# Kernel optimization log

Hardware: AMD Instinct MI355X
Metric: run time of the kernel (lower is better)

## Reference

```python
import jax, jax.numpy as jnp
import numpy as np

EMBED_DIM = 1024
NUM_HEADS = 16
HEAD_DIM = EMBED_DIM // NUM_HEADS
BZ, Q_LEN, CACHE_LEN = 4, 512, 1536


def setup_inputs() -> dict:
    key = jax.random.key(0)
    ks = jax.random.split(key, 8)
    inp = {
        "hidden_states": jax.random.normal(ks[0], (BZ, Q_LEN, EMBED_DIM), jnp.float32),
        "attention_mask": jnp.zeros((BZ, 1, 1, CACHE_LEN + Q_LEN), jnp.float32),
        "k_cache": jax.random.normal(ks[1], (BZ, CACHE_LEN, EMBED_DIM), jnp.float32),
        "v_cache": jax.random.normal(ks[2], (BZ, CACHE_LEN, EMBED_DIM), jnp.float32),
        "Wq": jax.random.normal(ks[3], (EMBED_DIM, EMBED_DIM), jnp.float32) * 0.02,
        "bq": jnp.zeros((EMBED_DIM,), jnp.float32),
        "Wk": jax.random.normal(ks[4], (EMBED_DIM, EMBED_DIM), jnp.float32) * 0.02,
        "bk": jnp.zeros((EMBED_DIM,), jnp.float32),
        "Wv": jax.random.normal(ks[5], (EMBED_DIM, EMBED_DIM), jnp.float32) * 0.02,
        "bv": jnp.zeros((EMBED_DIM,), jnp.float32),
        "Wo": jax.random.normal(ks[6], (EMBED_DIM, EMBED_DIM), jnp.float32) * 0.02,
        "bo": jnp.zeros((EMBED_DIM,), jnp.float32),
    }
    return inp


def reference(hidden_states, attention_mask, k_cache, v_cache,
              Wq, bq, Wk, bk, Wv, bv, Wo, bo):
    bz, q_len, embed_dim = hidden_states.shape
    # projections (nn.Linear: x @ W.T + b)
    q = hidden_states @ Wq.T + bq
    k_new = hidden_states @ Wk.T + bk
    v_new = hidden_states @ Wv.T + bv
    # KV-cache concat (self_attn path)
    k = jnp.concatenate([k_cache, k_new], axis=1)  # [bz, kv_len, E]
    v = jnp.concatenate([v_cache, v_new], axis=1)
    q_begin = k_cache.shape[1]
    kv_len = k.shape[1]
    # split heads -> [bz, H, L, D]
    qh = q.reshape(bz, q_len, NUM_HEADS, HEAD_DIM).transpose(0, 2, 1, 3)
    kh = k.reshape(bz, kv_len, NUM_HEADS, HEAD_DIM).transpose(0, 2, 1, 3)
    vh = v.reshape(bz, kv_len, NUM_HEADS, HEAD_DIM).transpose(0, 2, 1, 3)
    scores = jnp.einsum("bhqd,bhkd->bhqk", qh, kh) / (HEAD_DIM ** 0.5)
    # causal mask slice causal_mask[q_begin:q_begin+q_len, :kv_len]
    rows = q_begin + jnp.arange(q_len)          # absolute query positions
    cols = jnp.arange(kv_len)
    causal = jnp.where(cols[None, :] > rows[:, None], -jnp.inf, 0.0).astype(scores.dtype)
    scores = scores + attention_mask + causal
    probs = jax.nn.softmax(scores, axis=-1)
    ctx = jnp.einsum("bhqk,bhkd->bhqd", probs, vh)
    ctx = ctx.transpose(0, 2, 1, 3).reshape(bz, q_len, embed_dim)
    out = ctx @ Wo.T + bo
    return out, k, v
```

## Files before the change

### kernel.cpp

```cpp
#include <hip/hip_runtime.h>
#include <hip/hip_bf16.h>
#include <stdint.h>

#define BZv 4
#define QL 512
#define CL 1536
#define KVL 2048
#define EMB 1024
#define NH 16
#define HD 64
#define QSCALE 0.18033688011112042f

typedef __attribute__((ext_vector_type(8))) short short8;
typedef __attribute__((ext_vector_type(4))) float floatx4;

__device__ __forceinline__ unsigned short f2b(float f) {
  union { float f; unsigned int u; } v; v.f = f;
  return (unsigned short)((v.u + 0x7FFFu + ((v.u >> 16) & 1u)) >> 16);
}

__device__ __forceinline__ ushort2 pk2(float a, float b) {
  union { __hip_bfloat162 h; ushort2 u; } c;
  c.h = __float22bfloat162_rn(make_float2(a, b));
  return c.u;
}

#if __has_builtin(__builtin_amdgcn_exp2f)
#define EXP2F(x) __builtin_amdgcn_exp2f(x)
#else
#define EXP2F(x) exp2f(x)
#endif

__device__ __forceinline__ void gload_lds16(const void* g, void* l) {
  __builtin_amdgcn_global_load_lds(
      (const __attribute__((address_space(1))) unsigned char*)g,
      (__attribute__((address_space(3))) unsigned char*)l, 16, 0, 0);
}

__global__ __launch_bounds__(256) void prep_kernel(
    const float* __restrict__ hid, const float* __restrict__ Wq, const float* __restrict__ Wk,
    const float* __restrict__ Wv, const float* __restrict__ Wo,
    const float* __restrict__ kc, const float* __restrict__ vc, const float* __restrict__ msk,
    unsigned short* __restrict__ Xb, unsigned short* __restrict__ Wqb, unsigned short* __restrict__ Wkb,
    unsigned short* __restrict__ Wvb, unsigned short* __restrict__ Wob,
    unsigned short* __restrict__ Kb, unsigned short* __restrict__ Vb,
    float* __restrict__ kf, float* __restrict__ vf, unsigned short* __restrict__ wb)
{
  const long HID4 = (long)BZv * QL * EMB / 4;
  const long W4   = (long)EMB * EMB / 4;
  const long C4   = (long)BZv * CL * EMB / 4;
  const long t0 = HID4, t1 = t0 + W4, t2 = t1 + W4, t3 = t2 + W4, t4 = t3 + W4;
  const long t5 = t4 + C4, t6 = t5 + C4;
  const long total = t6 + (long)BZv * KVL / 4;
  for (long i = (long)blockIdx.x * blockDim.x + threadIdx.x; i < total;
       i += (long)gridDim.x * blockDim.x) {
    if (i < t4) {
      const float* src; unsigned short* dst; long j;
      if (i < t0)      { src = hid; dst = Xb;  j = i; }
      else if (i < t1) { src = Wq;  dst = Wqb; j = i - t0; }
      else if (i < t2) { src = Wk;  dst = Wkb; j = i - t1; }
      else if (i < t3) { src = Wv;  dst = Wvb; j = i - t2; }
      else             { src = Wo;  dst = Wob; j = i - t3; }
      float4 v = ((const float4*)src)[j];
      ushort4 o; o.x = f2b(v.x); o.y = f2b(v.y); o.z = f2b(v.z); o.w = f2b(v.w);
      ((ushort4*)dst)[j] = o;
    } else if (i < t6) {
      bool isV = (i >= t5);
      long j = i - (isV ? t5 : t4);
      const float* src = isV ? vc : kc;
      float4 v = ((const float4*)src)[j];
      long e4 = j * 4;
      int b = (int)(e4 / ((long)CL * EMB));
      long rem = e4 - (long)b * CL * EMB;
      long doff = (long)b * KVL * EMB + rem;
      if (isV) {
        *((float4*)(vf + doff)) = v;
        int row = (int)(rem >> 10);
        float w = __expf(msk[b * KVL + row]);
        ushort4 o; o.x = f2b(v.x * w); o.y = f2b(v.y * w);
        o.z = f2b(v.z * w); o.w = f2b(v.w * w);
        *((ushort4*)(Vb + doff)) = o;
      } else {
        *((float4*)(kf + doff)) = v;
        ushort4 o; o.x = f2b(v.x); o.y = f2b(v.y); o.z = f2b(v.z); o.w = f2b(v.w);
        *((ushort4*)(Kb + doff)) = o;
      }
    } else {
      long j = i - t6;
      float4 m4 = ((const float4*)msk)[j];
      ushort4 o;
      o.x = f2b(__expf(m4.x)); o.y = f2b(__expf(m4.y));
      o.z = f2b(__expf(m4.z)); o.w = f2b(__expf(m4.w));
      ((ushort4*)wb)[j] = o;
    }
  }
}

__global__ __launch_bounds__(256) void qkv_gemm(
    const unsigned short* __restrict__ Xb,
    const unsigned short* __restrict__ Wqb, const unsigned short* __restrict__ Wkb,
    const unsigned short* __restrict__ Wvb,
    const float* __restrict__ bq, const float* __restrict__ bk, const float* __restrict__ bv,
    const float* __restrict__ msk,
    unsigned short* __restrict__ Qb, unsigned short* __restrict__ Kb, unsigned short* __restrict__ Vb,
    float* __restrict__ kf, float* __restrict__ vf)
{
  __shared__ unsigned short At[128 * 32];
  __shared__ unsigned short Bt[64 * 32];
  const int tid = threadIdx.x, lane = tid & 63, wave = tid >> 6;
  const int quad = lane >> 4, l = lane & 15;
  const int mat = blockIdx.x >> 4;
  const int ncol = (blockIdx.x & 15) * 64;
  const int mbase = blockIdx.y * 128;
  const unsigned short* W = (mat == 0) ? Wqb : (mat == 1) ? Wkb : Wvb;
  const float* bias = (mat == 0) ? bq : (mat == 1) ? bk : bv;
  const int srow = tid >> 2, slds = tid & 3;
  const int rh = wave * 32;

  floatx4 zero = {0.f, 0.f, 0.f, 0.f};
  floatx4 acc[2][4];
#pragma unroll
  for (int i = 0; i < 2; i++)
#pragma unroll
    for (int j = 0; j < 4; j++) acc[i][j] = zero;

  for (int k0 = 0; k0 < EMB; k0 += 32) {
    __syncthreads();
#pragma unroll
    for (int s = 0; s < 2; s++) {
      int row = s * 64 + srow;
      int gc = slds ^ (row & 3);
      gload_lds16(Xb + (size_t)(mbase + row) * EMB + k0 + gc * 8, &At[row * 32 + slds * 8]);
    }
    {
      int row = srow;
      int gc = slds ^ (row & 3);
      gload_lds16(W + (size_t)(ncol + row) * EMB + k0 + gc * 8, &Bt[row * 32 + slds * 8]);
    }
    __syncthreads();
    short8 af[2], bfr[4];
#pragma unroll
    for (int rt = 0; rt < 2; rt++) {
      int row = rh + rt * 16 + l;
      af[rt] = *(const short8*)&At[row * 32 + ((quad ^ (row & 3)) * 8)];
    }
#pragma unroll
    for (int ct = 0; ct < 4; ct++) {
      int row = ct * 16 + l;
      bfr[ct] = *(const short8*)&Bt[row * 32 + ((quad ^ (row & 3)) * 8)];
    }
#pragma unroll
    for (int rt = 0; rt < 2; rt++)
#pragma unroll
      for (int ct = 0; ct < 4; ct++)
        acc[rt][ct] = __builtin_amdgcn_mfma_f32_16x16x32_bf16(af[rt], bfr[ct], acc[rt][ct], 0, 0, 0);
  }

#pragma unroll
  for (int ct = 0; ct < 4; ct++) {
    int col = ncol + ct * 16 + l;
    float bb = bias[col];
#pragma unroll
    for (int rt = 0; rt < 2; rt++)
#pragma unroll
      for (int r = 0; r < 4; r++) {
        int m = mbase + rh + rt * 16 + quad * 4 + r;
        float val = acc[rt][ct][r] + bb;
        if (mat == 0) {
          Qb[(size_t)m * EMB + col] = f2b(val * QSCALE);
        } else {
          size_t a = ((size_t)(m >> 9) * KVL + CL + (m & 511)) * EMB + col;
          if (mat == 1) { Kb[a] = f2b(val); kf[a] = val; }
          else {
            float w = __expf(msk[(m >> 9) * KVL + CL + (m & 511)]);
            Vb[a] = f2b(val * w); vf[a] = val;
          }
        }
      }
  }
}

__global__ __launch_bounds__(256) void oproj_gemm(
    const unsigned short* __restrict__ A, const unsigned short* __restrict__ W,
    const float* __restrict__ bias, float* __restrict__ out)
{
  __shared__ unsigned short At[64 * 32];
  __shared__ unsigned short Bt[64 * 32];
  const int tid = threadIdx.x, lane = tid & 63, wave = tid >> 6;
  const int quad = lane >> 4, l = lane & 15;
  const int ncol = blockIdx.x * 64;
  const int mbase = blockIdx.y * 64;
  const int srow = tid >> 2, slds = tid & 3;
  const int rh = (wave & 1) * 32, ch = (wave >> 1) * 32;

  floatx4 zero = {0.f, 0.f, 0.f, 0.f};
  floatx4 acc[2][2];
#pragma unroll
  for (int i = 0; i < 2; i++)
#pragma unroll
    for (int j = 0; j < 2; j++) acc[i][j] = zero;

  for (int k0 = 0; k0 < EMB; k0 += 32) {
    __syncthreads();
    {
      int gc = slds ^ (srow & 3);
      gload_lds16(A + (size_t)(mbase + srow) * EMB + k0 + gc * 8, &At[srow * 32 + slds * 8]);
      gload_lds16(W + (size_t)(ncol + srow) * EMB + k0 + gc * 8, &Bt[srow * 32 + slds * 8]);
    }
    __syncthreads();
    short8 af[2], bfr[2];
#pragma unroll
    for (int rt = 0; rt < 2; rt++) {
      int row = rh + rt * 16 + l;
      af[rt] = *(const short8*)&At[row * 32 + ((quad ^ (row & 3)) * 8)];
    }
#pragma unroll
    for (int ct = 0; ct < 2; ct++) {
      int row = ch + ct * 16 + l;
      bfr[ct] = *(const short8*)&Bt[row * 32 + ((quad ^ (row & 3)) * 8)];
    }
#pragma unroll
    for (int rt = 0; rt < 2; rt++)
#pragma unroll
      for (int ct = 0; ct < 2; ct++)
        acc[rt][ct] = __builtin_amdgcn_mfma_f32_16x16x32_bf16(af[rt], bfr[ct], acc[rt][ct], 0, 0, 0);
  }

#pragma unroll
  for (int ct = 0; ct < 2; ct++) {
    int col = ncol + ch + ct * 16 + l;
    float bb = bias[col];
#pragma unroll
    for (int rt = 0; rt < 2; rt++)
#pragma unroll
      for (int r = 0; r < 4; r++) {
        int m = mbase + rh + rt * 16 + quad * 4 + r;
        out[(size_t)m * EMB + col] = acc[rt][ct][r] + bb;
      }
  }
}

__global__ __launch_bounds__(256) void attn_kernel(
    const unsigned short* __restrict__ Qb, const unsigned short* __restrict__ Kb,
    const unsigned short* __restrict__ Vb, const unsigned short* __restrict__ wb,
    unsigned short* __restrict__ Cb)
{
  __shared__ unsigned short Vt[2][66 * 72];
  __shared__ unsigned short Pl[4][16 * 72];
  const int id = blockIdx.x;
  const int hb = id & 63, qt = id >> 6;
  const int b = hb >> 4, h = hb & 15;
  const int tid = threadIdx.x, lane = tid & 63, wave = tid >> 6;
  const int quad = lane >> 4, l = lane & 15;
  const int qbase = qt * 64 + wave * 16;

  const unsigned short* qp = Qb + (size_t)(b * QL + qbase + l) * EMB + h * HD + quad * 8;
  const short8 bq0 = *(const short8*)qp;
  const short8 bq1 = *(const short8*)(qp + 32);

  floatx4 zero = {0.f, 0.f, 0.f, 0.f};
  floatx4 o[4], o4 = zero;
#pragma unroll
  for (int c = 0; c < 4; c++) o[c] = zero;
  float mr = -INFINITY;

  const int kv_end = CL + qt * 64 + 64;
  const int vp = tid & 31, vg = tid >> 5;
  const unsigned short* vsrc = Vb + (size_t)(b * KVL) * EMB + h * HD + vg * 8;
  const unsigned short* wsrc = wb + (size_t)b * KVL + 2 * vp;
  const unsigned short* kbase = Kb + (size_t)(b * KVL) * EMB + h * HD + quad * 8;

  uint4 va = *(const uint4*)(vsrc + (size_t)(2 * vp) * EMB);
  uint4 vbr = *(const uint4*)(vsrc + (size_t)(2 * vp + 1) * EMB);
  short8 kc[8];
#pragma unroll
  for (int c = 0; c < 4; c++) {
    const unsigned short* kp = kbase + (size_t)(c * 16 + l) * EMB;
    kc[2 * c] = *(const short8*)kp;
    kc[2 * c + 1] = *(const short8*)(kp + 32);
  }
  {
    const unsigned short* pa = (const unsigned short*)&va;
    const unsigned short* pb = (const unsigned short*)&vbr;
#pragma unroll
    for (int j = 0; j < 8; j++) {
      ushort2 t; t.x = pa[j]; t.y = pb[j];
      *(ushort2*)&Vt[0][(vg * 8 + j) * 72 + 2 * vp] = t;
    }
    if (vg == 0) *(ushort2*)&Vt[0][64 * 72 + 2 * vp] = *(const ushort2*)wsrc;
  }
  __syncthreads();

  int cur = 0;
  for (int kv0 = 0; kv0 < kv_end; kv0 += 64) {
    const bool more = (kv0 + 64 < kv_end);
    uint4 vna, vnb; ushort2 wn; short8 kn[8];
    if (more) {
      const unsigned short* vs = vsrc + (size_t)(kv0 + 64 + 2 * vp) * EMB;
      vna = *(const uint4*)vs;
      vnb = *(const uint4*)(vs + EMB);
      if (vg == 0) wn = *(const ushort2*)(wsrc + kv0 + 64);
#pragma unroll
      for (int c = 0; c < 4; c++) {
        const unsigned short* kp = kbase + (size_t)(kv0 + 64 + c * 16 + l) * EMB;
        kn[2 * c] = *(const short8*)kp;
        kn[2 * c + 1] = *(const short8*)(kp + 32);
      }
    }
    floatx4 s[4];
#pragma unroll
    for (int c = 0; c < 4; c++) {
      s[c] = __builtin_amdgcn_mfma_f32_16x16x32_bf16(kc[2 * c], bq0, zero, 0, 0, 0);
      s[c] = __builtin_amdgcn_mfma_f32_16x16x32_bf16(kc[2 * c + 1], bq1, s[c], 0, 0, 0);
    }
    if (kv0 + 63 > CL + qbase) {
      const int lim = CL + qbase + l;
#pragma unroll
      for (int c = 0; c < 4; c++) {
        int kvb = kv0 + c * 16 + quad * 4;
#pragma unroll
        for (int r = 0; r < 4; r++)
          s[c][r] = (kvb + r <= lim) ? s[c][r] : -INFINITY;
      }
    }
    float t0 = fmaxf(fmaxf(s[0][0], s[0][1]), fmaxf(s[0][2], s[0][3]));
    float t1 = fmaxf(fmaxf(s[1][0], s[1][1]), fmaxf(s[1][2], s[1][3]));
    float t2 = fmaxf(fmaxf(s[2][0], s[2][1]), fmaxf(s[2][2], s[2][3]));
    float t3 = fmaxf(fmaxf(s[3][0], s[3][1]), fmaxf(s[3][2], s[3][3]));
    float lmax = fmaxf(fmaxf(t0, t1), fmaxf(t2, t3));
    lmax = fmaxf(lmax, __shfl_xor(lmax, 16, 64));
    lmax = fmaxf(lmax, __shfl_xor(lmax, 32, 64));
    float mnew = fmaxf(mr, lmax);
    float alpha = EXP2F(mr - mnew);
    mr = mnew;
#pragma unroll
    for (int c = 0; c < 4; c++) {
      float p0 = EXP2F(s[c][0] - mnew), p1 = EXP2F(s[c][1] - mnew);
      float p2 = EXP2F(s[c][2] - mnew), p3 = EXP2F(s[c][3] - mnew);
      ushort2 lo = pk2(p0, p1), hi = pk2(p2, p3);
      ushort4 pk; pk.x = lo.x; pk.y = lo.y; pk.z = hi.x; pk.w = hi.y;
      *(ushort4*)&Pl[wave][l * 72 + c * 16 + quad * 4] = pk;
    }
#pragma unroll
    for (int c = 0; c < 4; c++)
#pragma unroll
      for (int r = 0; r < 4; r++) o[c][r] *= alpha;
#pragma unroll
    for (int r = 0; r < 4; r++) o4[r] *= alpha;
    asm volatile("s_waitcnt lgkmcnt(0)" ::: "memory");
    short8 pf0 = *(const short8*)&Pl[wave][l * 72 + quad * 8];
    short8 pf1 = *(const short8*)&Pl[wave][l * 72 + 32 + quad * 8];
    short8 vw0 = *(const short8*)&Vt[cur][64 * 72 + quad * 8];
    short8 vw1 = *(const short8*)&Vt[cur][64 * 72 + 32 + quad * 8];
    o4 = __builtin_amdgcn_mfma_f32_16x16x32_bf16(vw0, pf0, o4, 0, 0, 0);
    o4 = __builtin_amdgcn_mfma_f32_16x16x32_bf16(vw1, pf1, o4, 0, 0, 0);
#pragma unroll
    for (int c = 0; c < 4; c++) {
      short8 a0v = *(const short8*)&Vt[cur][(c * 16 + l) * 72 + quad * 8];
      short8 a1v = *(const short8*)&Vt[cur][(c * 16 + l) * 72 + 32 + quad * 8];
      o[c] = __builtin_amdgcn_mfma_f32_16x16x32_bf16(a0v, pf0, o[c], 0, 0, 0);
      o[c] = __builtin_amdgcn_mfma_f32_16x16x32_bf16(a1v, pf1, o[c], 0, 0, 0);
    }
    if (more) {
      const unsigned short* pa = (const unsigned short*)&vna;
      const unsigned short* pb = (const unsigned short*)&vnb;
#pragma unroll
      for (int j = 0; j < 8; j++) {
        ushort2 t; t.x = pa[j]; t.y = pb[j];
        *(ushort2*)&Vt[cur ^ 1][(vg * 8 + j) * 72 + 2 * vp] = t;
      }
      if (vg == 0) *(ushort2*)&Vt[cur ^ 1][64 * 72 + 2 * vp] = wn;
#pragma unroll
      for (int i = 0; i < 8; i++) kc[i] = kn[i];
    }
    __syncthreads();
    cur ^= 1;
  }

  float inv = 1.0f / o4[0];
  size_t qrow = (size_t)(b * QL + qbase + l) * EMB + h * HD;
#pragma unroll
  for (int c = 0; c < 4; c++)
#pragma unroll
    for (int r = 0; r < 4; r++)
      Cb[qrow + c * 16 + quad * 4 + r] = f2b(o[c][r] * inv);
}

extern "C" void kernel_launch(void* const* d_in, const int* in_sizes, int n_in,
                              void* d_out, int out_size, void* d_ws, size_t ws_size,
                              hipStream_t stream) {
  const float* hid  = (const float*)d_in[0];
  const float* mask = (const float*)d_in[1];
  const float* kc   = (const float*)d_in[2];
  const float* vc   = (const float*)d_in[3];
  const float* Wq   = (const float*)d_in[4];
  const float* bq   = (const float*)d_in[5];
  const float* Wk   = (const float*)d_in[6];
  const float* bk   = (const float*)d_in[7];
  const float* Wv   = (const float*)d_in[8];
  const float* bv   = (const float*)d_in[9];
  const float* Wo   = (const float*)d_in[10];
  const float* bo   = (const float*)d_in[11];

  float* out_f = (float*)d_out;
  float* kf = out_f + (size_t)BZv * QL * EMB;
  float* vf = kf + (size_t)BZv * KVL * EMB;

  char* p = (char*)d_ws;
  unsigned short* Xb  = (unsigned short*)p; p += (size_t)BZv * QL * EMB * 2;
  unsigned short* Wqb = (unsigned short*)p; p += (size_t)EMB * EMB * 2;
  unsigned short* Wkb = (unsigned short*)p; p += (size_t)EMB * EMB * 2;
  unsigned short* Wvb = (unsigned short*)p; p += (size_t)EMB * EMB * 2;
  unsigned short* Wob = (unsigned short*)p; p += (size_t)EMB * EMB * 2;
  unsigned short* Qb  = (unsigned short*)p; p += (size_t)BZv * QL * EMB * 2;
  unsigned short* Kb  = (unsigned short*)p; p += (size_t)BZv * KVL * EMB * 2;
  unsigned short* Vb  = (unsigned short*)p; p += (size_t)BZv * KVL * EMB * 2;
  unsigned short* Cb  = (unsigned short*)p; p += (size_t)BZv * QL * EMB * 2;
  unsigned short* wbp = (unsigned short*)p; p += (size_t)BZv * KVL * 2;

  prep_kernel<<<2048, 256, 0, stream>>>(hid, Wq, Wk, Wv, Wo, kc, vc, mask,
                                        Xb, Wqb, Wkb, Wvb, Wob, Kb, Vb, kf, vf, wbp);
  qkv_gemm<<<dim3(48, 16), 256, 0, stream>>>(Xb, Wqb, Wkb, Wvb, bq, bk, bv, mask,
                                             Qb, Kb, Vb, kf, vf);
  attn_kernel<<<512, 256, 0, stream>>>(Qb, Kb, Vb, wbp, Cb);
  oproj_gemm<<<dim3(16, 32), 256, 0, stream>>>(Cb, Wob, bo, out_f);
}
```

Baseline: 287.8 us.

## Split-KV attention across waves, pre-transpose V, enlarge GEMM tiles

Attention now gives each block 16 query rows and splits the KV tiles across its four waves. Partial results are merged through shared memory with a log-sum-exp style rescale, which raises the grid from 512 to 2048 blocks. A new vtrans_kernel writes V (plus the mask-weight row) transposed per head into global memory, so the attention loop loads V fragments straight from global instead of transposing through LDS. The QKV and output-projection GEMMs move to larger 128-wide N tiles for more reuse. The costs are an extra kernel launch, an extra V round trip through memory, and more registers per thread.

New measurement: 325.8 us. 1.13x slower.

```diff
diff --git a/kernel.cpp b/kernel.cpp
--- a/kernel.cpp
+++ b/kernel.cpp
@@ -106,21 +106,21 @@
     float* __restrict__ kf, float* __restrict__ vf)
 {
   __shared__ unsigned short At[128 * 32];
-  __shared__ unsigned short Bt[64 * 32];
+  __shared__ unsigned short Bt[128 * 32];
   const int tid = threadIdx.x, lane = tid & 63, wave = tid >> 6;
   const int quad = lane >> 4, l = lane & 15;
-  const int mat = blockIdx.x >> 4;
-  const int ncol = (blockIdx.x & 15) * 64;
+  const int mat = blockIdx.x >> 3;
+  const int ncol = (blockIdx.x & 7) * 128;
   const int mbase = blockIdx.y * 128;
   const unsigned short* W = (mat == 0) ? Wqb : (mat == 1) ? Wkb : Wvb;
   const float* bias = (mat == 0) ? bq : (mat == 1) ? bk : bv;
   const int srow = tid >> 2, slds = tid & 3;
-  const int rh = wave * 32;
+  const int rh = (wave & 1) * 64, ch = (wave >> 1) * 64;
 
   floatx4 zero = {0.f, 0.f, 0.f, 0.f};
-  floatx4 acc[2][4];
-#pragma unroll
-  for (int i = 0; i < 2; i++)
+  floatx4 acc[4][4];
+#pragma unroll
+  for (int i = 0; i < 4; i++)
 #pragma unroll
     for (int j = 0; j < 4; j++) acc[i][j] = zero;
 
@@ -132,51 +132,88 @@
       int gc = slds ^ (row & 3);
       gload_lds16(Xb + (size_t)(mbase + row) * EMB + k0 + gc * 8, &At[row * 32 + slds * 8]);
     }
-    {
-      int row = srow;
+#pragma unroll
+    for (int s = 0; s < 2; s++) {
+      int row = s * 64 + srow;
       int gc = slds ^ (row & 3);
       gload_lds16(W + (size_t)(ncol + row) * EMB + k0 + gc * 8, &Bt[row * 32 + slds * 8]);
     }
     __syncthreads();
-    short8 af[2], bfr[4];
-#pragma unroll
-    for (int rt = 0; rt < 2; rt++) {
+    short8 af[4], bfr[4];
+#pragma unroll
+    for (int rt = 0; rt < 4; rt++) {
       int row = rh + rt * 16 + l;
       af[rt] = *(const short8*)&At[row * 32 + ((quad ^ (row & 3)) * 8)];
     }
 #pragma unroll
     for (int ct = 0; ct < 4; ct++) {
-      int row = ct * 16 + l;
+      int row = ch + ct * 16 + l;
       bfr[ct] = *(const short8*)&Bt[row * 32 + ((quad ^ (row & 3)) * 8)];
     }
 #pragma unroll
-    for (int rt = 0; rt < 2; rt++)
+    for (int rt = 0; rt < 4; rt++)
 #pragma unroll
       for (int ct = 0; ct < 4; ct++)
         acc[rt][ct] = __builtin_amdgcn_mfma_f32_16x16x32_bf16(af[rt], bfr[ct], acc[rt][ct], 0, 0, 0);
   }
 
 #pragma unroll
-  for (int ct = 0; ct < 4; ct++) {
-    int col = ncol + ct * 16 + l;
-    float bb = bias[col];
-#pragma unroll
-    for (int rt = 0; rt < 2; rt++)
-#pragma unroll
-      for (int r = 0; r < 4; r++) {
-        int m = mbase + rh + rt * 16 + quad * 4 + r;
-        float val = acc[rt][ct][r] + bb;
+  for (int rt = 0; rt < 4; rt++)
+#pragma unroll
+    for (int r = 0; r < 4; r++) {
+      int m = mbase + rh + rt * 16 + quad * 4 + r;
+      size_t orow; float w = 1.f;
+      if (mat == 0) orow = (size_t)m;
+      else {
+        orow = (size_t)(m >> 9) * KVL + CL + (m & 511);
+        if (mat == 2) w = __expf(msk[orow]);
+      }
+#pragma unroll
+      for (int ct = 0; ct < 4; ct++) {
+        int col = ncol + ch + ct * 16 + l;
+        float val = acc[rt][ct][r] + bias[col];
         if (mat == 0) {
           Qb[(size_t)m * EMB + col] = f2b(val * QSCALE);
         } else {
-          size_t a = ((size_t)(m >> 9) * KVL + CL + (m & 511)) * EMB + col;
+          size_t a = orow * EMB + col;
           if (mat == 1) { Kb[a] = f2b(val); kf[a] = val; }
-          else {
-            float w = __expf(msk[(m >> 9) * KVL + CL + (m & 511)]);
-            Vb[a] = f2b(val * w); vf[a] = val;
-          }
+          else          { Vb[a] = f2b(val * w); vf[a] = val; }
         }
       }
+    }
+}
+
+__global__ __launch_bounds__(256) void vtrans_kernel(
+    const unsigned short* __restrict__ Vb, const unsigned short* __restrict__ wb,
+    unsigned short* __restrict__ Vtg)
+{
+  __shared__ unsigned short T[64 * 72];
+  const int id = blockIdx.x;
+  const int bh = id & 63, kt = id >> 6;
+  const int b = bh >> 4, h = bh & 15;
+  const int kv0 = kt * 64;
+  const int tid = threadIdx.x;
+  {
+    const int r = tid >> 2, dbase = (tid & 3) * 16;
+    const unsigned short* src = Vb + (size_t)(b * KVL + kv0 + r) * EMB + h * HD + dbase;
+    uint4 lo = *(const uint4*)src;
+    uint4 hi = *(const uint4*)(src + 8);
+    *(uint4*)&T[r * 72 + dbase] = lo;
+    *(uint4*)&T[r * 72 + dbase + 8] = hi;
+  }
+  __syncthreads();
+  {
+    const int d = tid >> 2, kcv = (tid & 3) * 16;
+    unsigned short tmp[16];
+#pragma unroll
+    for (int j = 0; j < 16; j++) tmp[j] = T[(kcv + j) * 72 + d];
+    unsigned short* dst = Vtg + ((size_t)bh * 65 + d) * KVL + kv0 + kcv;
+    *(uint4*)dst = *(const uint4*)&tmp[0];
+    *(uint4*)(dst + 8) = *(const uint4*)&tmp[8];
+  }
+  if (tid < 16) {
+    ushort4 wv = *(const ushort4*)(wb + (size_t)b * KVL + kv0 + tid * 4);
+    *(ushort4*)(Vtg + ((size_t)bh * 65 + 64) * KVL + kv0 + tid * 4) = wv;
   }
 }
 
@@ -185,49 +222,54 @@
     const float* __restrict__ bias, float* __restrict__ out)
 {
   __shared__ unsigned short At[64 * 32];
-  __shared__ unsigned short Bt[64 * 32];
+  __shared__ unsigned short Bt[128 * 32];
   const int tid = threadIdx.x, lane = tid & 63, wave = tid >> 6;
   const int quad = lane >> 4, l = lane & 15;
-  const int ncol = blockIdx.x * 64;
+  const int ncol = blockIdx.x * 128;
   const int mbase = blockIdx.y * 64;
   const int srow = tid >> 2, slds = tid & 3;
-  const int rh = (wave & 1) * 32, ch = (wave >> 1) * 32;
+  const int rh = (wave & 1) * 32, ch = (wave >> 1) * 64;
 
   floatx4 zero = {0.f, 0.f, 0.f, 0.f};
-  floatx4 acc[2][2];
+  floatx4 acc[2][4];
 #pragma unroll
   for (int i = 0; i < 2; i++)
 #pragma unroll
-    for (int j = 0; j < 2; j++) acc[i][j] = zero;
+    for (int j = 0; j < 4; j++) acc[i][j] = zero;
 
   for (int k0 = 0; k0 < EMB; k0 += 32) {
     __syncthreads();
     {
       int gc = slds ^ (srow & 3);
       gload_lds16(A + (size_t)(mbase + srow) * EMB + k0 + gc * 8, &At[srow * 32 + slds * 8]);
-      gload_lds16(W + (size_t)(ncol + srow) * EMB + k0 + gc * 8, &Bt[srow * 32 + slds * 8]);
+    }
+#pragma unroll
+    for (int s = 0; s < 2; s++) {
+      int row = s * 64 + srow;
+      int gc = slds ^ (row & 3);
+      gload_lds16(W + (size_t)(ncol + row) * EMB + k0 + gc * 8, &Bt[row * 32 + slds * 8]);
     }
     __syncthreads();
-    short8 af[2], bfr[2];
+    short8 af[2], bfr[4];
 #pragma unroll
     for (int rt = 0; rt < 2; rt++) {
       int row = rh + rt * 16 + l;
       af[rt] = *(const short8*)&At[row * 32 + ((quad ^ (row & 3)) * 8)];
     }
 #pragma unroll
-    for (int ct = 0; ct < 2; ct++) {
+    for (int ct = 0; ct < 4; ct++) {
       int row = ch + ct * 16 + l;
       bfr[ct] = *(const short8*)&Bt[row * 32 + ((quad ^ (row & 3)) * 8)];
     }
 #pragma unroll
     for (int rt = 0; rt < 2; rt++)
 #pragma unroll
-      for (int ct = 0; ct < 2; ct++)
+      for (int ct = 0; ct < 4; ct++)
         acc[rt][ct] = __builtin_amdgcn_mfma_f32_16x16x32_bf16(af[rt], bfr[ct], acc[rt][ct], 0, 0, 0);
   }
 
 #pragma unroll
-  for (int ct = 0; ct < 2; ct++) {
+  for (int ct = 0; ct < 4; ct++) {
     int col = ncol + ch + ct * 16 + l;
     float bb = bias[col];
 #pragma unroll
@@ -242,79 +284,57 @@
 
 __global__ __launch_bounds__(256) void attn_kernel(
     const unsigned short* __restrict__ Qb, const unsigned short* __restrict__ Kb,
-    const unsigned short* __restrict__ Vb, const unsigned short* __restrict__ wb,
-    unsigned short* __restrict__ Cb)
+    const unsigned short* __restrict__ Vtg, unsigned short* __restrict__ Cb)
 {
-  __shared__ unsigned short Vt[2][66 * 72];
   __shared__ unsigned short Pl[4][16 * 72];
+  __shared__ float cmb[4][16][68];
   const int id = blockIdx.x;
-  const int hb = id & 63, qt = id >> 6;
-  const int b = hb >> 4, h = hb & 15;
+  const int bh = id & 63, qt = id >> 6;
+  const int b = bh >> 4, h = bh & 15;
   const int tid = threadIdx.x, lane = tid & 63, wave = tid >> 6;
   const int quad = lane >> 4, l = lane & 15;
-  const int qbase = qt * 64 + wave * 16;
-
-  const unsigned short* qp = Qb + (size_t)(b * QL + qbase + l) * EMB + h * HD + quad * 8;
+  const int q0 = qt * 16;
+
+  const unsigned short* qp = Qb + (size_t)(b * QL + q0 + l) * EMB + h * HD + quad * 8;
   const short8 bq0 = *(const short8*)qp;
   const short8 bq1 = *(const short8*)(qp + 32);
 
+  const unsigned short* kbase = Kb + (size_t)(b * KVL) * EMB + h * HD + quad * 8;
+  const unsigned short* vtb = Vtg + (size_t)bh * 65 * KVL;
+
   floatx4 zero = {0.f, 0.f, 0.f, 0.f};
   floatx4 o[4], o4 = zero;
 #pragma unroll
   for (int c = 0; c < 4; c++) o[c] = zero;
   float mr = -INFINITY;
 
-  const int kv_end = CL + qt * 64 + 64;
-  const int vp = tid & 31, vg = tid >> 5;
-  const unsigned short* vsrc = Vb + (size_t)(b * KVL) * EMB + h * HD + vg * 8;
-  const unsigned short* wsrc = wb + (size_t)b * KVL + 2 * vp;
-  const unsigned short* kbase = Kb + (size_t)(b * KVL) * EMB + h * HD + quad * 8;
-
-  uint4 va = *(const uint4*)(vsrc + (size_t)(2 * vp) * EMB);
-  uint4 vbr = *(const uint4*)(vsrc + (size_t)(2 * vp + 1) * EMB);
-  short8 kc[8];
-#pragma unroll
-  for (int c = 0; c < 4; c++) {
-    const unsigned short* kp = kbase + (size_t)(c * 16 + l) * EMB;
-    kc[2 * c] = *(const short8*)kp;
-    kc[2 * c + 1] = *(const short8*)(kp + 32);
-  }
-  {
-    const unsigned short* pa = (const unsigned short*)&va;
-    const unsigned short* pb = (const unsigned short*)&vbr;
-#pragma unroll
-    for (int j = 0; j < 8; j++) {
-      ushort2 t; t.x = pa[j]; t.y = pb[j];
-      *(ushort2*)&Vt[0][(vg * 8 + j) * 72 + 2 * vp] = t;
-    }
-    if (vg == 0) *(ushort2*)&Vt[0][64 * 72 + 2 * vp] = *(const ushort2*)wsrc;
-  }
-  __syncthreads();
-
-  int cur = 0;
-  for (int kv0 = 0; kv0 < kv_end; kv0 += 64) {
-    const bool more = (kv0 + 64 < kv_end);
-    uint4 vna, vnb; ushort2 wn; short8 kn[8];
-    if (more) {
-      const unsigned short* vs = vsrc + (size_t)(kv0 + 64 + 2 * vp) * EMB;
-      vna = *(const uint4*)vs;
-      vnb = *(const uint4*)(vs + EMB);
-      if (vg == 0) wn = *(const ushort2*)(wsrc + kv0 + 64);
-#pragma unroll
-      for (int c = 0; c < 4; c++) {
-        const unsigned short* kp = kbase + (size_t)(kv0 + 64 + c * 16 + l) * EMB;
-        kn[2 * c] = *(const short8*)kp;
-        kn[2 * c + 1] = *(const short8*)(kp + 32);
-      }
-    }
+  const int kv_end = CL + q0 + 16;
+  const int ntiles = (kv_end + 63) >> 6;
+
+  for (int t = wave; t < ntiles; t += 4) {
+    const int kv0 = t * 64;
+    short8 kc0[4], kc1[4], av0[4], av1[4];
+#pragma unroll
+    for (int c = 0; c < 4; c++) {
+      const unsigned short* kp = kbase + (size_t)(kv0 + c * 16 + l) * EMB;
+      kc0[c] = *(const short8*)kp;
+      kc1[c] = *(const short8*)(kp + 32);
+      const unsigned short* vpr = vtb + (size_t)(c * 16 + l) * KVL + kv0 + quad * 8;
+      av0[c] = *(const short8*)vpr;
+      av1[c] = *(const short8*)(vpr + 32);
+    }
+    const unsigned short* wpr = vtb + (size_t)64 * KVL + kv0 + quad * 8;
+    const short8 vw0 = *(const short8*)wpr;
+    const short8 vw1 = *(const short8*)(wpr + 32);
+
     floatx4 s[4];
 #pragma unroll
     for (int c = 0; c < 4; c++) {
-      s[c] = __builtin_amdgcn_mfma_f32_16x16x32_bf16(kc[2 * c], bq0, zero, 0, 0, 0);
-      s[c] = __builtin_amdgcn_mfma_f32_16x16x32_bf16(kc[2 * c + 1], bq1, s[c], 0, 0, 0);
-    }
-    if (kv0 + 63 > CL + qbase) {
-      const int lim = CL + qbase + l;
+      s[c] = __builtin_amdgcn_mfma_f32_16x16x32_bf16(kc0[c], bq0, zero, 0, 0, 0);
+      s[c] = __builtin_amdgcn_mfma_f32_16x16x32_bf16(kc1[c], bq1, s[c], 0, 0, 0);
+    }
+    if (kv0 + 63 >= kv_end) {
+      const int lim = CL + q0 + l;
 #pragma unroll
       for (int c = 0; c < 4; c++) {
         int kvb = kv0 + c * 16 + quad * 4;
@@ -350,40 +370,41 @@
     asm volatile("s_waitcnt lgkmcnt(0)" ::: "memory");
     short8 pf0 = *(const short8*)&Pl[wave][l * 72 + quad * 8];
     short8 pf1 = *(const short8*)&Pl[wave][l * 72 + 32 + quad * 8];
-    short8 vw0 = *(const short8*)&Vt[cur][64 * 72 + quad * 8];
-    short8 vw1 = *(const short8*)&Vt[cur][64 * 72 + 32 + quad * 8];
     o4 = __builtin_amdgcn_mfma_f32_16x16x32_bf16(vw0, pf0, o4, 0, 0, 0);
     o4 = __builtin_amdgcn_mfma_f32_16x16x32_bf16(vw1, pf1, o4, 0, 0, 0);
 #pragma unroll
     for (int c = 0; c < 4; c++) {
-      short8 a0v = *(const short8*)&Vt[cur][(c * 16 + l) * 72 + quad * 8];
-      short8 a1v = *(const short8*)&Vt[cur][(c * 16 + l) * 72 + 32 + quad * 8];
-      o[c] = __builtin_amdgcn_mfma_f32_16x16x32_bf16(a0v, pf0, o[c], 0, 0, 0);
-      o[c] = __builtin_amdgcn_mfma_f32_16x16x32_bf16(a1v, pf1, o[c], 0, 0, 0);
-    }
-    if (more) {
-      const unsigned short* pa = (const unsigned short*)&vna;
-      const unsigned short* pb = (const unsigned short*)&vnb;
-#pragma unroll
-      for (int j = 0; j < 8; j++) {
-        ushort2 t; t.x = pa[j]; t.y = pb[j];
-        *(ushort2*)&Vt[cur ^ 1][(vg * 8 + j) * 72 + 2 * vp] = t;
-      }
-      if (vg == 0) *(ushort2*)&Vt[cur ^ 1][64 * 72 + 2 * vp] = wn;
-#pragma unroll
-      for (int i = 0; i < 8; i++) kc[i] = kn[i];
-    }
-    __syncthreads();
-    cur ^= 1;
-  }
-
-  float inv = 1.0f / o4[0];
-  size_t qrow = (size_t)(b * QL + qbase + l) * EMB + h * HD;
+      o[c] = __builtin_amdgcn_mfma_f32_16x16x32_bf16(av0[c], pf0, o[c], 0, 0, 0);
+      o[c] = __builtin_amdgcn_mfma_f32_16x16x32_bf16(av1[c], pf1, o[c], 0, 0, 0);
+    }
+  }
+
 #pragma unroll
   for (int c = 0; c < 4; c++)
-#pragma unroll
-    for (int r = 0; r < 4; r++)
-      Cb[qrow + c * 16 + quad * 4 + r] = f2b(o[c][r] * inv);
+    *(float4*)&cmb[wave][l][c * 16 + quad * 4] = *(float4*)&o[c];
+  if (quad == 0) { cmb[wave][l][64] = mr; cmb[wave][l][65] = o4[0]; }
+  __syncthreads();
+
+  {
+    const int q = tid >> 4, dc = (tid & 15) * 4;
+    float m0 = cmb[0][q][64], m1 = cmb[1][q][64], m2 = cmb[2][q][64], m3 = cmb[3][q][64];
+    float mstar = fmaxf(fmaxf(m0, m1), fmaxf(m2, m3));
+    float s0 = EXP2F(m0 - mstar), s1 = EXP2F(m1 - mstar);
+    float s2 = EXP2F(m2 - mstar), s3 = EXP2F(m3 - mstar);
+    float den = s0 * cmb[0][q][65] + s1 * cmb[1][q][65] +
+                s2 * cmb[2][q][65] + s3 * cmb[3][q][65];
+    float4 a0 = *(float4*)&cmb[0][q][dc];
+    float4 a1 = *(float4*)&cmb[1][q][dc];
+    float4 a2 = *(float4*)&cmb[2][q][dc];
+    float4 a3 = *(float4*)&cmb[3][q][dc];
+    float inv = 1.0f / den;
+    float r0 = (s0 * a0.x + s1 * a1.x + s2 * a2.x + s3 * a3.x) * inv;
+    float r1 = (s0 * a0.y + s1 * a1.y + s2 * a2.y + s3 * a3.y) * inv;
+    float r2 = (s0 * a0.z + s1 * a1.z + s2 * a2.z + s3 * a3.z) * inv;
+    float r3 = (s0 * a0.w + s1 * a1.w + s2 * a2.w + s3 * a3.w) * inv;
+    ushort4 outv; outv.x = f2b(r0); outv.y = f2b(r1); outv.z = f2b(r2); outv.w = f2b(r3);
+    *(ushort4*)(Cb + (size_t)(b * QL + q0 + q) * EMB + h * HD + dc) = outv;
+  }
 }
 
 extern "C" void kernel_launch(void* const* d_in, const int* in_sizes, int n_in,
@@ -417,11 +438,13 @@
   unsigned short* Vb  = (unsigned short*)p; p += (size_t)BZv * KVL * EMB * 2;
   unsigned short* Cb  = (unsigned short*)p; p += (size_t)BZv * QL * EMB * 2;
   unsigned short* wbp = (unsigned short*)p; p += (size_t)BZv * KVL * 2;
+  unsigned short* Vtg = (unsigned short*)p; p += (size_t)NH * BZv * 65 * KVL * 2;
 
   prep_kernel<<<2048, 256, 0, stream>>>(hid, Wq, Wk, Wv, Wo, kc, vc, mask,
                                         Xb, Wqb, Wkb, Wvb, Wob, Kb, Vb, kf, vf, wbp);
-  qkv_gemm<<<dim3(48, 16), 256, 0, stream>>>(Xb, Wqb, Wkb, Wvb, bq, bk, bv, mask,
+  qkv_gemm<<<dim3(24, 16), 256, 0, stream>>>(Xb, Wqb, Wkb, Wvb, bq, bk, bv, mask,
                                              Qb, Kb, Vb, kf, vf);
-  attn_kernel<<<512, 256, 0, stream>>>(Qb, Kb, Vb, wbp, Cb);
-  oproj_gemm<<<dim3(16, 32), 256, 0, stream>>>(Cb, Wob, bo, out_f);
-}
+  vtrans_kernel<<<2048, 256, 0, stream>>>(Vb, wbp, Vtg);
+  attn_kernel<<<2048, 256, 0, stream>>>(Qb, Kb, Vtg, Cb);
+  oproj_gemm<<<dim3(8, 32), 256, 0, stream>>>(Cb, Wob, bo, out_f);
+}
```
